# Optimization experiments

Hardware: AMD Instinct MI355X
Metric: run time of the kernel (lower is better)

Reference implementation:

```python
import math
import jax, jax.numpy as jnp
import numpy as np

NUM_CLASSES = 80
CONF_THR = 0.05
IOU_THR = 0.5
MAX_PER_CLASS = 100
MAX_DET = 100
PRE_NMS_K = 200  # per-class candidates kept before greedy NMS (>= max_per_class)
BOX_VAR = np.array([0.1, 0.1, 0.2, 0.2], np.float32)
IMG_H, IMG_W = 640, 640
BATCH = 8


def _anchor_dims():
    ratios = [0.5, 1.0, 2.0]
    scales = [2.0 ** x for x in (0.0, 1.0 / 3.0, 2.0 / 3.0)]
    dims_all = []
    for area in [32.0 ** 2, 64.0 ** 2, 128.0 ** 2, 256.0 ** 2, 512.0 ** 2]:
        dims = []
        for r in ratios:  # ratio-major, scale-minor (matches AnchorBox._compute_dims)
            h = math.sqrt(area / r)
            w = area / h
            for s in scales:
                dims.append([s * w, s * h])
        dims_all.append(np.array(dims, np.float32))  # [9, 2]
    return dims_all


def get_anchors(H, W):
    """Anchors in [cx, cy, w, h], shape [total_anchors, 4] (static, numpy)."""
    strides = [8, 16, 32, 64, 128]
    out = []
    for stride, dims in zip(strides, _anchor_dims()):
        fh, fw = math.ceil(H / stride), math.ceil(W / stride)
        rx = (np.arange(fw, dtype=np.float32) + 0.5) * stride
        ry = (np.arange(fh, dtype=np.float32) + 0.5) * stride
        cx, cy = np.meshgrid(rx, ry)  # each [fh, fw], 'xy' indexing like tf.meshgrid
        centers = np.broadcast_to(np.stack([cx, cy], -1)[:, :, None, :], (fh, fw, 9, 2))
        d = np.broadcast_to(dims[None, None], (fh, fw, 9, 2))
        out.append(np.concatenate([centers, d], -1).reshape(-1, 4))
    return jnp.asarray(np.concatenate(out, 0))


def decode_boxes(anchors, box_pred):
    """Apply variance scaling + anchor offsets, return corner boxes."""
    b = box_pred * jnp.asarray(BOX_VAR)
    xy = b[..., :2] * anchors[..., 2:] + anchors[..., :2]
    wh = jnp.exp(b[..., 2:]) * anchors[..., 2:]
    return jnp.concatenate([xy - wh * 0.5, xy + wh * 0.5], axis=-1)


def pairwise_iou(b):
    lt = jnp.maximum(b[:, None, :2], b[None, :, :2])
    rb = jnp.minimum(b[:, None, 2:], b[None, :, 2:])
    wh = jnp.maximum(rb - lt, 0.0)
    inter = wh[..., 0] * wh[..., 1]
    area = (b[:, 2] - b[:, 0]) * (b[:, 3] - b[:, 1])
    return inter / (area[:, None] + area[None, :] - inter + 1e-8)


def nms_one_class(boxes, scores):
    """Greedy NMS over top PRE_NMS_K candidates for one class."""
    sc, idx = jax.lax.top_k(scores, PRE_NMS_K)
    bb = boxes[idx]  # [K, 4]
    valid = sc > CONF_THR
    iou = jax.lax.stop_gradient(pairwise_iou(bb))  # [K, K]
    ar = jnp.arange(PRE_NMS_K)

    def body(i, keep):
        supp = keep[i] & (iou[i] > IOU_THR) & (ar > i)
        return keep & ~supp

    keep = jax.lax.fori_loop(0, PRE_NMS_K, body, valid)
    sc = jnp.where(keep, sc, 0.0)
    sc2, j = jax.lax.top_k(sc, MAX_PER_CLASS)
    bb2 = jnp.where((sc2 > 0.0)[:, None], bb[j], 0.0)
    return bb2, sc2


def detect_one_image(boxes, cls_scores):
    """boxes [A,4] shared across classes, cls_scores [A,C]."""
    cb, cs = jax.vmap(nms_one_class, in_axes=(None, 1))(boxes, cls_scores)  # [C,100,4],[C,100]
    cls_id = jnp.broadcast_to(
        jnp.arange(NUM_CLASSES, dtype=jnp.float32)[:, None], cs.shape
    )
    flat_s = cs.reshape(-1)
    flat_b = cb.reshape(-1, 4)
    flat_c = cls_id.reshape(-1)
    s, i = jax.lax.top_k(flat_s, MAX_DET)
    b = jnp.where((s > 0.0)[:, None], flat_b[i], 0.0)
    c = jnp.where(s > 0.0, flat_c[i], 0.0)
    n = jnp.sum(s > 0.0).astype(jnp.int32)
    return b, s, c, n


def setup_inputs() -> dict:
    key = jax.random.key(0)
    k1, _ = jax.random.split(key)
    images = jnp.zeros((BATCH, IMG_H, IMG_W, 3), jnp.float32)  # only shape is used
    num_anchors = 76725  # 640x640 image -> (6400+1600+400+100+25)*9
    predictions = jax.random.normal(k1, (BATCH, num_anchors, 4 + NUM_CLASSES), jnp.float32)
    return {"images": images, "predictions": predictions}


def reference(images, predictions):
    H, W = images.shape[1], images.shape[2]
    anchors = get_anchors(H, W)  # [A, 4]
    box_pred = predictions[:, :, :4]
    cls_pred = jax.nn.sigmoid(predictions[:, :, 4:])  # [B, A, C]
    boxes = decode_boxes(anchors[None], box_pred)  # [B, A, 4]
    nmsed_boxes, nmsed_scores, nmsed_classes, valid = jax.vmap(detect_one_image)(
        boxes, cls_pred
    )
    return nmsed_boxes, nmsed_scores, nmsed_classes, valid
```

## Files before the change

kernel.cpp:

```cpp
#include <hip/hip_runtime.h>
#include <stdint.h>

typedef unsigned long long u64;
typedef unsigned int u32;
typedef unsigned char u8;

#define NB 8
#define NA 76725
#define NC 80
#define NCH 84
#define PRE_K 200
#define MAXPC 100
#define MAXDET 100
#define F4_PER_IMG (NA * 21u)

#define T0 0.93f
#define XCUT 2.58f
#define BLKX 256
#define SPAN (BLKX * 256u)
#define NSTEP 24
#define LCAP 24
#define CAP2 512
#define CAPF 2048


__device__ __forceinline__ float sigmoid_ref(float x) {
    return 1.0f / (1.0f + expf(-x));
}

__device__ void decode_box(float4 d, int a, float4* box, float* areaOut) {
    int lvl, off, fw, stride;
    if (a < 57600)      { lvl = 0; off = 0;     fw = 80; stride = 8;   }
    else if (a < 72000) { lvl = 1; off = 57600; fw = 40; stride = 16;  }
    else if (a < 75600) { lvl = 2; off = 72000; fw = 20; stride = 32;  }
    else if (a < 76500) { lvl = 3; off = 75600; fw = 10; stride = 64;  }
    else                { lvl = 4; off = 76500; fw = 5;  stride = 128; }
    int idx  = a - off;
    int k    = idx % 9;
    int cell = idx / 9;
    int row = cell / fw, col = cell - row * fw;
    float cx = __fmul_rn((float)col + 0.5f, (float)stride);
    float cy = __fmul_rn((float)row + 0.5f, (float)stride);
    int ri = k / 3, si = k - ri * 3;
    double r    = (ri == 0) ? 0.5 : ((ri == 1) ? 1.0 : 2.0);
    double side = (double)(32 << lvl);
    double area = side * side;
    double h = sqrt(area / r);
    double w = area / h;
    double s = exp2((double)si / 3.0);
    float aw = (float)(s * w);
    float ah = (float)(s * h);
    float b0 = __fmul_rn(d.x, 0.1f);
    float b1 = __fmul_rn(d.y, 0.1f);
    float b2 = __fmul_rn(d.z, 0.2f);
    float b3 = __fmul_rn(d.w, 0.2f);
    float ux = __fadd_rn(__fmul_rn(b0, aw), cx);
    float uy = __fadd_rn(__fmul_rn(b1, ah), cy);
    float wx = __fmul_rn(expf(b2), aw);
    float wy = __fmul_rn(expf(b3), ah);
    float hx = __fmul_rn(wx, 0.5f);
    float hy = __fmul_rn(wy, 0.5f);
    float x1 = __fsub_rn(ux, hx), y1 = __fsub_rn(uy, hy);
    float x2 = __fadd_rn(ux, hx), y2 = __fadd_rn(uy, hy);
    *box = make_float4(x1, y1, x2, y2);
    *areaOut = __fmul_rn(__fsub_rn(x2, x1), __fsub_rn(y2, y1));
}


__device__ __forceinline__ void scan4(float4 v, u32 idx,
                                      u32* lhist, u64 (*llist)[LCAP]) {
    u32 a  = idx / 21u;
    u32 c4 = idx - a * 21u;
    if (c4 == 0u) return;
    float m = fmaxf(fmaxf(v.x, v.y), fmaxf(v.z, v.w));
    if (m <= XCUT) return;
    u32 cb = c4 * 4u - 4u;
    float vv[4] = {v.x, v.y, v.z, v.w};
#pragma unroll
    for (int q = 0; q < 4; ++q) {
        if (vv[q] > XCUT) {
            float sig = sigmoid_ref(vv[q]);
            if (sig > T0) {
                u32 c = cb + (u32)q;
                u64 key = ((u64)__float_as_uint(sig) << 32) | (u64)(~a);
                u32 p = atomicAdd(&lhist[c], 1u);
                if (p < LCAP) llist[c][p] = key;
            }
        }
    }
}

__global__ __launch_bounds__(256, 4) void k_scan(const float4* __restrict__ p4,
                                                 u64* __restrict__ seg,
                                                 u32* __restrict__ cntT) {
    __shared__ u32 lhist[NC];
    __shared__ u64 llist[NC][LCAP];
    u32 b = blockIdx.y, x = blockIdx.x;
    for (u32 c = threadIdx.x; c < NC; c += 256u) lhist[c] = 0u;
    __syncthreads();

    const float4* base = p4 + (u64)b * F4_PER_IMG;
    u32 i0 = x * 256u + threadIdx.x;
#pragma unroll 1
    for (int s = 0; s < NSTEP; s += 4) {
        u32 ia = i0 + (u32)s * SPAN;
        float4 v0 = base[ia];
        float4 v1 = base[ia + SPAN];
        float4 v2 = base[ia + 2u * SPAN];
        float4 v3 = base[ia + 3u * SPAN];
        scan4(v0, ia,            lhist, llist);
        scan4(v1, ia + SPAN,     lhist, llist);
        scan4(v2, ia + 2u*SPAN,  lhist, llist);
        scan4(v3, ia + 3u*SPAN,  lhist, llist);
    }
    {
        u32 it = i0 + (u32)NSTEP * SPAN;
        if (it < F4_PER_IMG) scan4(base[it], it, lhist, llist);
    }
    __syncthreads();

    if (threadIdx.x < NC) {
        u32 c = threadIdx.x;
        u32 n = lhist[c];
        u32 m = n < LCAP ? n : (u32)LCAP;
        u64* o = seg + ((u64)(b * NC + c) * BLKX + x) * LCAP;
        for (u32 j = 0; j < m; ++j) o[j] = llist[c][j];
        cntT[(b * NC + c) * BLKX + x] = n;
    }
}


__global__ __launch_bounds__(256) void k_nms(const float* __restrict__ pred,
                                             const u64* __restrict__ seg,
                                             const u32* __restrict__ cntT,
                                             float* __restrict__ sc2,
                                             float* __restrict__ bb2) {
    int bc = blockIdx.x;
    int b = bc / NC, c = bc % NC;
    __shared__ u64 keys[CAP2];
    __shared__ u64 sorted[PRE_K];
    __shared__ u32 wsum[4];
    __shared__ u32 oflow[4];
    __shared__ float4 box[PRE_K];
    __shared__ u32 rsupA[PRE_K][8];
    __shared__ u32 validw[8];
    __shared__ u32 keepw[8];
    __shared__ u64 red[256];

    u32 tid = threadIdx.x, lane = tid & 63u, wv = tid >> 6;

    u32 n_raw = cntT[(u64)bc * BLKX + tid];
    u32 m_c = n_raw < LCAP ? n_raw : (u32)LCAP;
    u32 v = m_c;
#pragma unroll
    for (u32 d = 1; d < 64u; d <<= 1) {
        u32 t = __shfl_up(v, d, 64);
        if (lane >= d) v += t;
    }
    u64 ob = __ballot(n_raw > (u32)LCAP);
    if (lane == 63u) wsum[wv] = v;
    if (lane == 0u)  oflow[wv] = (ob != 0ull) ? 1u : 0u;
    __syncthreads();
    u32 off = 0;
    for (u32 w = 0; w < wv; ++w) off += wsum[w];
    u32 inc = v + off;
    u32 total = wsum[0] + wsum[1] + wsum[2] + wsum[3];
    bool over = (oflow[0] | oflow[1] | oflow[2] | oflow[3]) != 0u;
    bool repaired = over || (total < (u32)PRE_K) || (total > (u32)CAP2);

    if (!repaired) {
        u32 dst = inc - m_c;
        const u64* src = seg + ((u64)bc * BLKX + tid) * LCAP;
        for (u32 j = 0; j < m_c; ++j) keys[dst + j] = src[j];
        __syncthreads();
        u64 ka = (tid < total) ? keys[tid] : 0ull;
        u64 kb = (tid + 256u < total) ? keys[tid + 256u] : 0ull;
        u32 ra = 0, rb = 0;
        for (u32 j = 0; j < total; ++j) {
            u64 kj = keys[j];
            ra += (kj > ka) ? 1u : 0u;
            rb += (kj > kb) ? 1u : 0u;
        }
        if (tid < total && ra < (u32)PRE_K) sorted[ra] = ka;
        if (tid + 256u < total && rb < (u32)PRE_K) sorted[rb] = kb;
        __syncthreads();
    } else {
        u64 cur = ~0ull;
        for (int k = 0; k < PRE_K; ++k) {
            u64 loc = 0;
            for (int a = tid; a < NA; a += 256) {
                float xx = pred[((long)b * NA + a) * NCH + 4 + c];
                float sg = sigmoid_ref(xx);
                u64 key  = ((u64)__float_as_uint(sg) << 32) | (u64)(~(u32)a);
                if (key < cur && key > loc) loc = key;
            }
            red[tid] = loc;
            __syncthreads();
            for (int s = 128; s > 0; s >>= 1) {
                if (tid < (u32)s) {
                    if (red[tid + s] > red[tid]) red[tid] = red[tid + s];
                }
                __syncthreads();
            }
            cur = red[0];
            if (tid == 0) sorted[k] = cur;
            __syncthreads();
        }
    }

    bool val = false;
    float4 mybox = make_float4(0.f, 0.f, 0.f, 0.f);
    float myarea = 0.f;
    if (tid < (u32)PRE_K) {
        u64 key = sorted[tid];
        float sig = __uint_as_float((u32)(key >> 32));
        int a = (int)(~(u32)key);
        if (sig > 0.05f) {
            float4 dd = *(const float4*)(pred + ((long)b * NA + a) * NCH);
            decode_box(dd, a, &mybox, &myarea);
            val = true;
        }
        box[tid] = mybox;
    }
    u64 vbal = __ballot(val);
    if (lane == 0u) {
        validw[2u * wv]      = (u32)vbal;
        validw[2u * wv + 1u] = (u32)(vbal >> 32);
    }
    __syncthreads();

    u32 rsup[7];
#pragma unroll
    for (int w = 0; w < 7; ++w) {
        u32 m = 0;
        if (val && (u32)(w * 32) < tid) {
            for (int ii = 0; ii < 32; ++ii) {
                int i = w * 32 + ii;
                if ((u32)i < tid) {
                    float4 bi = box[i];
                    float ai = __fmul_rn(__fsub_rn(bi.z, bi.x), __fsub_rn(bi.w, bi.y));
                    float ltx = fmaxf(bi.x, mybox.x), lty = fmaxf(bi.y, mybox.y);
                    float rbx = fminf(bi.z, mybox.z), rby = fminf(bi.w, mybox.w);
                    float wx = fmaxf(__fsub_rn(rbx, ltx), 0.f);
                    float wy = fmaxf(__fsub_rn(rby, lty), 0.f);
                    float inter = __fmul_rn(wx, wy);
                    float den = __fadd_rn(__fsub_rn(__fadd_rn(ai, myarea), inter), 1e-8f);
                    float iou = __fdiv_rn(inter, den);
                    if (iou > 0.5f) m |= 1u << ii;
                }
            }
        }
        rsup[w] = m;
    }
    if (tid < (u32)PRE_K) {
#pragma unroll
        for (int w = 0; w < 7; ++w) rsupA[tid][w] = rsup[w];
        rsupA[tid][7] = 0u;
    }
    __syncthreads();

    if (tid < 64u) {
        u32 l = tid;
        uint4 sA0 = *(const uint4*)&rsupA[l][0];
        uint4 sA1 = *(const uint4*)&rsupA[l][4];
        uint4 sB0 = *(const uint4*)&rsupA[l + 64u][0];
        uint4 sB1 = *(const uint4*)&rsupA[l + 64u][4];
        uint4 sC0 = *(const uint4*)&rsupA[l + 128u][0];
        uint4 sC1 = *(const uint4*)&rsupA[l + 128u][4];
        uint4 sD0 = make_uint4(0u, 0u, 0u, 0u);
        uint4 sD1 = make_uint4(0u, 0u, 0u, 0u);
        if (l < 8u) {
            sD0 = *(const uint4*)&rsupA[l + 192u][0];
            sD1 = *(const uint4*)&rsupA[l + 192u][4];
        }
        u32 v0 = validw[0], v1 = validw[1], v2 = validw[2], v3 = validw[3];
        u32 v4 = validw[4], v5 = validw[5], v6 = validw[6];
        u32 vb0 = (u32)(((((u64)v1 << 32) | v0) >> l) & 1ull);
        u32 vb1 = (u32)(((((u64)v3 << 32) | v2) >> l) & 1ull);
        u32 vb2 = (u32)(((((u64)v5 << 32) | v4) >> l) & 1ull);
        u32 vb3 = (l < 8u) ? ((v6 >> l) & 1u) : 0u;
        u32 k0 = v0, k1 = v1, k2 = v2, k3 = v3, k4 = v4, k5 = v5, k6 = v6;
        for (int t = 0; t < PRE_K; ++t) {
            u32 s0 = (k0 & sA0.x) | (k1 & sA0.y) | (k2 & sA0.z) | (k3 & sA0.w)
                   | (k4 & sA1.x) | (k5 & sA1.y) | (k6 & sA1.z);
            u32 s1 = (k0 & sB0.x) | (k1 & sB0.y) | (k2 & sB0.z) | (k3 & sB0.w)
                   | (k4 & sB1.x) | (k5 & sB1.y) | (k6 & sB1.z);
            u32 s2 = (k0 & sC0.x) | (k1 & sC0.y) | (k2 & sC0.z) | (k3 & sC0.w)
                   | (k4 & sC1.x) | (k5 & sC1.y) | (k6 & sC1.z);
            u32 s3 = (k0 & sD0.x) | (k1 & sD0.y) | (k2 & sD0.z) | (k3 & sD0.w)
                   | (k4 & sD1.x) | (k5 & sD1.y) | (k6 & sD1.z);
            bool n0 = vb0 && (s0 == 0u);
            bool n1 = vb1 && (s1 == 0u);
            bool n2 = vb2 && (s2 == 0u);
            bool n3 = (vb3 != 0u) && (s3 == 0u);
            u64 B0 = __ballot(n0), B1 = __ballot(n1), B2 = __ballot(n2), B3 = __ballot(n3);
            u32 nk0 = (u32)B0, nk1 = (u32)(B0 >> 32);
            u32 nk2 = (u32)B1, nk3 = (u32)(B1 >> 32);
            u32 nk4 = (u32)B2, nk5 = (u32)(B2 >> 32);
            u32 nk6 = (u32)B3;
            bool same = (nk0 == k0) && (nk1 == k1) && (nk2 == k2) && (nk3 == k3)
                     && (nk4 == k4) && (nk5 == k5) && (nk6 == k6);
            k0 = nk0; k1 = nk1; k2 = nk2; k3 = nk3; k4 = nk4; k5 = nk5; k6 = nk6;
            if (same) break;
        }
        if (l == 0u) {
            keepw[0] = k0; keepw[1] = k1; keepw[2] = k2; keepw[3] = k3;
            keepw[4] = k4; keepw[5] = k5; keepw[6] = k6;
        }
    }
    __syncthreads();

    int kept = 0;
#pragma unroll
    for (int w = 0; w < 7; ++w) kept += __popc(keepw[w]);
    if (kept > MAXPC) kept = MAXPC;

    if (tid >= (u32)kept && tid < (u32)MAXPC) {
        int pos = tid;
        sc2[bc * MAXPC + pos] = 0.f;
        float* o = bb2 + ((long)bc * MAXPC + pos) * 4;
        o[0] = 0.f; o[1] = 0.f; o[2] = 0.f; o[3] = 0.f;
    }
    if (tid < (u32)PRE_K) {
        int r = tid;
        if ((keepw[r >> 5] >> (r & 31)) & 1u) {
            int pos = 0;
            for (int w = 0; w < (r >> 5); ++w) pos += __popc(keepw[w]);
            pos += __popc(keepw[r >> 5] & ((1u << (r & 31)) - 1u));
            if (pos < MAXPC) {
                u64 key = sorted[r];
                float sig = __uint_as_float((u32)(key >> 32));
                sc2[bc * MAXPC + pos] = sig;
                float* o = bb2 + ((long)bc * MAXPC + pos) * 4;
                o[0] = mybox.x; o[1] = mybox.y; o[2] = mybox.z; o[3] = mybox.w;
            }
        }
    }
}


__global__ __launch_bounds__(1024) void k_final(const float* __restrict__ sc2,
                                                const float* __restrict__ bb2,
                                                float* __restrict__ out) {
    int b = blockIdx.x;
    __shared__ u32 hist[256];
    __shared__ u32 sfx[256];
    __shared__ u64 keys[CAPF];
    __shared__ u64 top[128];
    __shared__ u32 cnt_s;
    __shared__ int t_s;
    __shared__ u64 red[1024];

    for (int i = threadIdx.x; i < 256; i += blockDim.x) hist[i] = 0u;
    if (threadIdx.x < 128) top[threadIdx.x] = 0ull;
    if (threadIdx.x == 0) { cnt_s = 0u; t_s = 0; }
    __syncthreads();

    const float* s_b = sc2 + b * (NC * MAXPC);
    for (int f = threadIdx.x; f < NC * MAXPC; f += blockDim.x) {
        float s = s_b[f];
        if (s > 0.f) {
            int bin = (int)(s * 256.f); if (bin > 255) bin = 255;
            atomicAdd(&hist[bin], 1u);
        }
    }
    __syncthreads();

    if (threadIdx.x < 256) sfx[threadIdx.x] = hist[threadIdx.x];
    __syncthreads();
    for (u32 d = 1; d < 256u; d <<= 1) {
        u32 v = 0;
        if (threadIdx.x < 256u && threadIdx.x + d < 256u) v = sfx[threadIdx.x + d];
        __syncthreads();
        if (threadIdx.x < 256u) sfx[threadIdx.x] += v;
        __syncthreads();
    }
    if (threadIdx.x < 256) {
        bool ge = sfx[threadIdx.x] >= (u32)MAXDET;
        bool nlt = (threadIdx.x == 255) || (sfx[threadIdx.x + 1] < (u32)MAXDET);
        if (ge && nlt) t_s = (int)threadIdx.x;
    }
    __syncthreads();
    int t = t_s;

    for (int f = threadIdx.x; f < NC * MAXPC; f += blockDim.x) {
        float s = s_b[f];
        if (s > 0.f) {
            int bin = (int)(s * 256.f); if (bin > 255) bin = 255;
            if (bin >= t) {
                u32 pos = atomicAdd(&cnt_s, 1u);
                if (pos < CAPF)
                    keys[pos] = ((u64)__float_as_uint(s) << 32) | (u64)(~(u32)f);
            }
        }
    }
    __syncthreads();
    u32 g = cnt_s;

    if (g <= (u32)CAPF) {
        u64 ka = (threadIdx.x < g) ? keys[threadIdx.x] : 0ull;
        u64 kb = (threadIdx.x + 1024u < g) ? keys[threadIdx.x + 1024u] : 0ull;
        u32 ra = 0, rb = 0;
        for (u32 j = 0; j < g; ++j) {
            u64 kj = keys[j];
            ra += (kj > ka) ? 1u : 0u;
            rb += (kj > kb) ? 1u : 0u;
        }
        if (threadIdx.x < g && ra < (u32)MAXDET) top[ra] = ka;
        if (threadIdx.x + 1024u < g && rb < (u32)MAXDET) top[rb] = kb;
        __syncthreads();
    } else {
        u64 cur = ~0ull;
        for (int k = 0; k < MAXDET; ++k) {
            u64 loc = 0;
            for (int f = threadIdx.x; f < NC * MAXPC; f += blockDim.x) {
                float s = s_b[f];
                if (s > 0.f) {
                    u64 key = ((u64)__float_as_uint(s) << 32) | (u64)(~(u32)f);
                    if (key < cur && key > loc) loc = key;
                }
            }
            red[threadIdx.x] = loc;
            __syncthreads();
            for (int st = 512; st > 0; st >>= 1) {
                if (threadIdx.x < (u32)st) {
                    if (red[threadIdx.x + st] > red[threadIdx.x])
                        red[threadIdx.x] = red[threadIdx.x + st];
                }
                __syncthreads();
            }
            cur = red[0];
            if (threadIdx.x == 0) top[k] = cur;
            __syncthreads();
        }
        if (threadIdx.x == 0) {
            u32 nv = 0;
            for (int r = 0; r < MAXDET; ++r) if (top[r] != 0ull) ++nv;
            cnt_s = nv;
        }
        __syncthreads();
        g = cnt_s;
    }

    if (threadIdx.x < MAXDET) {
        int r = threadIdx.x;
        u64 key = top[r];
        u32 hi = (u32)(key >> 32);
        float s = 0.f, cf = 0.f;
        float bx0 = 0.f, bx1 = 0.f, bx2 = 0.f, bx3 = 0.f;
        if (hi != 0u) {
            s = __uint_as_float(hi);
            int f = (int)(~(u32)key);
            int c = f / MAXPC, jj = f - c * MAXPC;
            const float* bsrc = bb2 + ((long)(b * NC + c) * MAXPC + jj) * 4;
            bx0 = bsrc[0]; bx1 = bsrc[1]; bx2 = bsrc[2]; bx3 = bsrc[3];
            cf = (float)c;
        }
        float* ob = out + ((long)b * MAXDET + r) * 4;
        ob[0] = bx0; ob[1] = bx1; ob[2] = bx2; ob[3] = bx3;
        out[NB * MAXDET * 4 + b * MAXDET + r] = s;
        out[NB * MAXDET * 4 + NB * MAXDET + b * MAXDET + r] = cf;
    }
    if (threadIdx.x == 0) {
        u32 nv = g < (u32)MAXDET ? g : (u32)MAXDET;
        out[NB * MAXDET * 4 + 2 * NB * MAXDET + b] = (float)nv;
    }
}


extern "C" void kernel_launch(void* const* d_in, const int* in_sizes, int n_in,
                              void* d_out, int out_size, void* d_ws, size_t ws_size,
                              hipStream_t stream) {
    const float* pred = (const float*)d_in[1];
    if (n_in >= 2 && in_sizes[0] == NB * NA * NCH) pred = (const float*)d_in[0];

    char* ws = (char*)d_ws;
    const long BCN = (long)NB * NC;
    u64* seg   = (u64*)ws;
    char* p    = ws + BCN * BLKX * LCAP * 8;
    u32* cntT  = (u32*)p;            p += BCN * BLKX * 4;
    float* sc2 = (float*)p;          p += BCN * MAXPC * 4;
    float* bb2 = (float*)p;

    k_scan <<<dim3(BLKX, NB), 256, 0, stream>>>((const float4*)pred, seg, cntT);
    k_nms  <<<dim3(NB * NC),  256, 0, stream>>>(pred, seg, cntT, sc2, bb2);
    k_final<<<dim3(NB),      1024, 0, stream>>>(sc2, bb2, (float*)d_out);
}
```

Before: 110.8 us.

## Parallelize NMS IoU matrix over pairs with 512-thread blocks and shared atomics

Raises k_nms to 512 threads and replaces the per-row triangular IoU loop, where thread i did up to 200 serial IoU checks, with a flat loop over all box pairs spread across the block. Suppression bits are set with shared-memory atomicOr into a zero-initialized matrix. The rank sort now gives one key per thread instead of two. The aim is to shorten the imbalanced serial IoU work. The cost is twice the pairs evaluated (the full square, with half skipped), integer division per pair, shared atomics, and an extra zeroing pass and barrier.

```diff
diff --git a/kernel.cpp b/kernel.cpp
--- a/kernel.cpp
+++ b/kernel.cpp
@@ -130,7 +130,7 @@
 }
 
 
-__global__ __launch_bounds__(256) void k_nms(const float* __restrict__ pred,
+__global__ __launch_bounds__(512) void k_nms(const float* __restrict__ pred,
                                              const u64* __restrict__ seg,
                                              const u32* __restrict__ cntT,
                                              float* __restrict__ sc2,
@@ -145,50 +145,52 @@
     __shared__ u32 rsupA[PRE_K][8];
     __shared__ u32 validw[8];
     __shared__ u32 keepw[8];
-    __shared__ u64 red[256];
+    __shared__ u64 red[512];
 
     u32 tid = threadIdx.x, lane = tid & 63u, wv = tid >> 6;
 
-    u32 n_raw = cntT[(u64)bc * BLKX + tid];
-    u32 m_c = n_raw < LCAP ? n_raw : (u32)LCAP;
-    u32 v = m_c;
+    u32 m_c = 0, incv = 0;
+    if (tid < 256u) {
+        u32 n_raw = cntT[(u64)bc * BLKX + tid];
+        m_c = n_raw < LCAP ? n_raw : (u32)LCAP;
+        u32 v = m_c;
 #pragma unroll
-    for (u32 d = 1; d < 64u; d <<= 1) {
-        u32 t = __shfl_up(v, d, 64);
-        if (lane >= d) v += t;
-    }
-    u64 ob = __ballot(n_raw > (u32)LCAP);
-    if (lane == 63u) wsum[wv] = v;
-    if (lane == 0u)  oflow[wv] = (ob != 0ull) ? 1u : 0u;
-    __syncthreads();
-    u32 off = 0;
-    for (u32 w = 0; w < wv; ++w) off += wsum[w];
-    u32 inc = v + off;
+        for (u32 d = 1; d < 64u; d <<= 1) {
+            u32 t = __shfl_up(v, d, 64);
+            if (lane >= d) v += t;
+        }
+        u64 ob = __ballot(n_raw > (u32)LCAP);
+        if (lane == 63u) wsum[wv] = v;
+        if (lane == 0u)  oflow[wv] = (ob != 0ull) ? 1u : 0u;
+        incv = v;
+    }
+    __syncthreads();
     u32 total = wsum[0] + wsum[1] + wsum[2] + wsum[3];
     bool over = (oflow[0] | oflow[1] | oflow[2] | oflow[3]) != 0u;
     bool repaired = over || (total < (u32)PRE_K) || (total > (u32)CAP2);
 
     if (!repaired) {
-        u32 dst = inc - m_c;
-        const u64* src = seg + ((u64)bc * BLKX + tid) * LCAP;
-        for (u32 j = 0; j < m_c; ++j) keys[dst + j] = src[j];
+        if (tid < 256u) {
+            u32 off = 0;
+            for (u32 w = 0; w < wv; ++w) off += wsum[w];
+            u32 dst = incv + off - m_c;
+            const u64* src = seg + ((u64)bc * BLKX + tid) * LCAP;
+            for (u32 j = 0; j < m_c; ++j) keys[dst + j] = src[j];
+        }
         __syncthreads();
         u64 ka = (tid < total) ? keys[tid] : 0ull;
-        u64 kb = (tid + 256u < total) ? keys[tid + 256u] : 0ull;
-        u32 ra = 0, rb = 0;
+        u32 ra = 0;
         for (u32 j = 0; j < total; ++j) {
             u64 kj = keys[j];
             ra += (kj > ka) ? 1u : 0u;
-            rb += (kj > kb) ? 1u : 0u;
         }
         if (tid < total && ra < (u32)PRE_K) sorted[ra] = ka;
-        if (tid + 256u < total && rb < (u32)PRE_K) sorted[rb] = kb;
         __syncthreads();
     } else {
         u64 cur = ~0ull;
         for (int k = 0; k < PRE_K; ++k) {
             u64 loc = 0;
-            for (int a = tid; a < NA; a += 256) {
+            for (int a = tid; a < NA; a += 512) {
                 float xx = pred[((long)b * NA + a) * NCH + 4 + c];
                 float sg = sigmoid_ref(xx);
                 u64 key  = ((u64)__float_as_uint(sg) << 32) | (u64)(~(u32)a);
@@ -196,7 +198,7 @@
             }
             red[tid] = loc;
             __syncthreads();
-            for (int s = 128; s > 0; s >>= 1) {
+            for (int s = 256; s > 0; s >>= 1) {
                 if (tid < (u32)s) {
                     if (red[tid + s] > red[tid]) red[tid] = red[tid + s];
                 }
@@ -208,54 +210,47 @@
         }
     }
 
+    for (u32 i = tid; i < (u32)PRE_K * 8u; i += 512u) rsupA[i >> 3][i & 7u] = 0u;
+    if (tid < 8u) validw[tid] = 0u;
+    __syncthreads();
+
     bool val = false;
     float4 mybox = make_float4(0.f, 0.f, 0.f, 0.f);
-    float myarea = 0.f;
     if (tid < (u32)PRE_K) {
         u64 key = sorted[tid];
         float sig = __uint_as_float((u32)(key >> 32));
         int a = (int)(~(u32)key);
         if (sig > 0.05f) {
             float4 dd = *(const float4*)(pred + ((long)b * NA + a) * NCH);
-            decode_box(dd, a, &mybox, &myarea);
+            float ar;
+            decode_box(dd, a, &mybox, &ar);
             val = true;
         }
         box[tid] = mybox;
     }
     u64 vbal = __ballot(val);
-    if (lane == 0u) {
+    if (lane == 0u && wv < 4u) {
         validw[2u * wv]      = (u32)vbal;
         validw[2u * wv + 1u] = (u32)(vbal >> 32);
     }
     __syncthreads();
 
-    u32 rsup[7];
-#pragma unroll
-    for (int w = 0; w < 7; ++w) {
-        u32 m = 0;
-        if (val && (u32)(w * 32) < tid) {
-            for (int ii = 0; ii < 32; ++ii) {
-                int i = w * 32 + ii;
-                if ((u32)i < tid) {
-                    float4 bi = box[i];
-                    float ai = __fmul_rn(__fsub_rn(bi.z, bi.x), __fsub_rn(bi.w, bi.y));
-                    float ltx = fmaxf(bi.x, mybox.x), lty = fmaxf(bi.y, mybox.y);
-                    float rbx = fminf(bi.z, mybox.z), rby = fminf(bi.w, mybox.w);
-                    float wx = fmaxf(__fsub_rn(rbx, ltx), 0.f);
-                    float wy = fmaxf(__fsub_rn(rby, lty), 0.f);
-                    float inter = __fmul_rn(wx, wy);
-                    float den = __fadd_rn(__fsub_rn(__fadd_rn(ai, myarea), inter), 1e-8f);
-                    float iou = __fdiv_rn(inter, den);
-                    if (iou > 0.5f) m |= 1u << ii;
-                }
-            }
-        }
-        rsup[w] = m;
-    }
-    if (tid < (u32)PRE_K) {
-#pragma unroll
-        for (int w = 0; w < 7; ++w) rsupA[tid][w] = rsup[w];
-        rsupA[tid][7] = 0u;
+    for (u32 p = tid; p < (u32)(PRE_K * PRE_K); p += 512u) {
+        u32 i  = p / (u32)PRE_K;
+        u32 jx = p - i * (u32)PRE_K;
+        if (jx > i) {
+            float4 bi = box[i], bj = box[jx];
+            float ai = __fmul_rn(__fsub_rn(bi.z, bi.x), __fsub_rn(bi.w, bi.y));
+            float aj = __fmul_rn(__fsub_rn(bj.z, bj.x), __fsub_rn(bj.w, bj.y));
+            float ltx = fmaxf(bi.x, bj.x), lty = fmaxf(bi.y, bj.y);
+            float rbx = fminf(bi.z, bj.z), rby = fminf(bi.w, bj.w);
+            float wx = fmaxf(__fsub_rn(rbx, ltx), 0.f);
+            float wy = fmaxf(__fsub_rn(rby, lty), 0.f);
+            float inter = __fmul_rn(wx, wy);
+            float den = __fadd_rn(__fsub_rn(__fadd_rn(ai, aj), inter), 1e-8f);
+            float iou = __fdiv_rn(inter, den);
+            if (iou > 0.5f) atomicOr(&rsupA[jx][i >> 5], 1u << (i & 31u));
+        }
     }
     __syncthreads();
 
@@ -483,6 +478,6 @@
     float* bb2 = (float*)p;
 
     k_scan <<<dim3(BLKX, NB), 256, 0, stream>>>((const float4*)pred, seg, cntT);
-    k_nms  <<<dim3(NB * NC),  256, 0, stream>>>(pred, seg, cntT, sc2, bb2);
+    k_nms  <<<dim3(NB * NC),  512, 0, stream>>>(pred, seg, cntT, sc2, bb2);
     k_final<<<dim3(NB),      1024, 0, stream>>>(sc2, bb2, (float*)d_out);
 }
```

Result: faster. 104.1 us (-6.0%).
